# Performance work log

Measured on AMD Instinct MI355X. Metric: run time of the kernel, lower is better.

Reference implementation:

```python
import jax, jax.numpy as jnp
import numpy as np

HID = 101
IN = 3


def lstm_cell(x, h, c, W_ih, W_hh, b_ih, b_hh):
    # PyTorch LSTMCell gate order: i, f, g, o
    gates = x @ W_ih.T + b_ih + h @ W_hh.T + b_hh  # [B, 4H]
    i, f, g, o = jnp.split(gates, 4, axis=-1)
    i = jax.nn.sigmoid(i)
    f = jax.nn.sigmoid(f)
    g = jnp.tanh(g)
    o = jax.nn.sigmoid(o)
    c_new = f * c + i * g
    h_new = o * jnp.tanh(c_new)
    return h_new, c_new


def setup_inputs() -> dict:
    key = jax.random.key(0)
    ks = jax.random.split(key, 12)
    B, T = 1024, 256
    s1 = 1.0 / np.sqrt(HID)
    u = lambda k, shp: jax.random.uniform(k, shp, jnp.float32, -s1, s1)
    return {
        "input": jax.random.normal(ks[0], (B, T, IN), jnp.float32),
        "W_ih1": u(ks[1], (4 * HID, IN)),
        "W_hh1": u(ks[2], (4 * HID, HID)),
        "b_ih1": u(ks[3], (4 * HID,)),
        "b_hh1": u(ks[4], (4 * HID,)),
        "W_ih2": u(ks[5], (4 * HID, HID)),
        "W_hh2": u(ks[6], (4 * HID, HID)),
        "b_ih2": u(ks[7], (4 * HID,)),
        "b_hh2": u(ks[8], (4 * HID,)),
        "Wl": u(ks[9], (IN, HID)),
        "bl": u(ks[10], (IN,)),
        "future": 32,
    }


def reference(input, W_ih1, W_hh1, b_ih1, b_hh1, W_ih2, W_hh2, b_ih2, b_hh2, Wl, bl, future):
    B = input.shape[0]
    h1 = jnp.zeros((B, HID), input.dtype)
    c1 = jnp.zeros((B, HID), input.dtype)
    h2 = jnp.zeros((B, HID), input.dtype)
    c2 = jnp.zeros((B, HID), input.dtype)

    def step(carry, x_t):
        h1, c1, h2, c2 = carry
        h1, c1 = lstm_cell(x_t, h1, c1, W_ih1, W_hh1, b_ih1, b_hh1)
        h2, c2 = lstm_cell(h1, h2, c2, W_ih2, W_hh2, b_ih2, b_hh2)
        out = h2 @ Wl.T + bl  # [B, 3]
        return (h1, c1, h2, c2), out

    xs = jnp.transpose(input, (1, 0, 2))  # [T, B, 3]
    carry, outs = jax.lax.scan(step, (h1, c1, h2, c2), xs)

    if future > 0:
        last_out = outs[-1]

        def fstep(carry, _):
            h1, c1, h2, c2, out = carry
            h1, c1 = lstm_cell(out, h1, c1, W_ih1, W_hh1, b_ih1, b_hh1)
            h2, c2 = lstm_cell(h1, h2, c2, W_ih2, W_hh2, b_ih2, b_hh2)
            out = h2 @ Wl.T + bl
            return (h1, c1, h2, c2, out), out

        _, fouts = jax.lax.scan(fstep, (*carry, last_out), None, length=future)
        outs = jnp.concatenate([outs, fouts], axis=0)

    return jnp.transpose(outs, (1, 0, 2))  # [B, T+future, 3]
```

## Files before the change

kernel.cpp:

```cpp
#include <hip/hip_runtime.h>
#include <hip/hip_bf16.h>

#define HID 101
#define BATCH 1024
#define RPB 4
#define NBLK 256
#define NTHR 512
#define TSEQ 256

#define A1SZ  (7*4*4*512)
#define A2SZ  (7*4*7*512)
#define A2OFF A1SZ
#define AOOFF (A1SZ + A2SZ)
#define AOSZ  (4*512)

typedef _Float16 h8 __attribute__((ext_vector_type(8)));
typedef float f4 __attribute__((ext_vector_type(4)));

__global__ void prep_kernel(const float* __restrict__ W_ih1, const float* __restrict__ W_hh1,
                            const float* __restrict__ b_ih1, const float* __restrict__ b_hh1,
                            const float* __restrict__ W_ih2, const float* __restrict__ W_hh2,
                            const float* __restrict__ b_ih2, const float* __restrict__ b_hh2,
                            const float* __restrict__ Wl, _Float16* __restrict__ wsA) {
    int idx = blockIdx.x * blockDim.x + threadIdx.x;
    int stride = gridDim.x * blockDim.x;
    for (int t = idx; t < A1SZ; t += stride) {
        int i = t & 7, lane = (t >> 3) & 63, kt = (t >> 9) & 3, tau = (t >> 11) & 3, w = t >> 13;
        int k = kt * 32 + ((lane >> 4) & 3) * 8 + i;
        int u = 16 * w + (lane & 15);
        float v = 0.f;
        if (u < HID) {
            int g = tau * HID + u;
            if (k < HID) v = W_hh1[g * HID + k];
            else if (k >= 101 && k <= 103) v = W_ih1[g * 3 + (k - 101)];
            else if (k == 104) v = b_ih1[g] + b_hh1[g];
        }
        wsA[t] = (_Float16)v;
    }
    for (int t = idx; t < A2SZ; t += stride) {
        int i = t & 7, lane = (t >> 3) & 63;
        int rem = t >> 9;
        int kt = rem % 7; rem /= 7;
        int tau = rem & 3, w = rem >> 2;
        int k = kt * 32 + ((lane >> 4) & 3) * 8 + i;
        int u = 16 * w + (lane & 15);
        float v = 0.f;
        if (u < HID) {
            int g = tau * HID + u;
            if (k < HID) v = W_ih2[g * HID + k];
            else if (k == 104) v = b_ih2[g] + b_hh2[g];
            else if (k >= 112 && k < 213) v = W_hh2[g * HID + (k - 112)];
        }
        wsA[A2OFF + t] = (_Float16)v;
    }
    for (int t = idx; t < AOSZ; t += stride) {
        int i = t & 7, lane = (t >> 3) & 63, kk = (t >> 9) & 3;
        int k = (kk + 3) * 32 + ((lane >> 4) & 3) * 8 + i;
        int j = lane & 15;
        float v = (j < 3 && k >= 112 && k < 213) ? Wl[j * HID + (k - 112)] : 0.f;
        wsA[AOOFF + t] = (_Float16)v;
    }
}

__device__ __forceinline__ float sigm(float z) {
    return __builtin_amdgcn_rcpf(1.f + __expf(-z));
}
__device__ __forceinline__ float tanhf_(float z) {
    return 1.f - 2.f * __builtin_amdgcn_rcpf(__expf(2.f * z) + 1.f);
}

#define MFMA(acc, a, b) acc = __builtin_amdgcn_mfma_f32_16x16x32_f16(a, b, acc, 0, 0, 0)

__global__ __launch_bounds__(NTHR, 2) void lstm_kernel(
    const float* __restrict__ input, const _Float16* __restrict__ wsA,
    const float* __restrict__ bl, int steps, float* __restrict__ out)
{
    const int tid = threadIdx.x;
    const int wid = tid >> 6, lane = tid & 63;
    const int q = lane >> 4, col = lane & 15;
    const int r0 = blockIdx.x * RPB;
    const int ostride = steps * 3;

    __shared__ _Float16 Sb[2][3584];
    __shared__ float zwA[7][4][4][16];
    __shared__ float zwB[7][4][4][16];
    __shared__ _Float16 xpre[TSEQ * 12];

    h8 A1[4][4];
    h8 A2[4][7];
    if (wid < 7) {
        #pragma unroll
        for (int tau = 0; tau < 4; tau++) {
            #pragma unroll
            for (int kt = 0; kt < 4; kt++)
                A1[tau][kt] = *(const volatile h8*)(
                    wsA + ((size_t)((wid * 4 + tau) * 4 + kt) * 512 + lane * 8));
            #pragma unroll
            for (int kt = 0; kt < 7; kt++)
                A2[tau][kt] = *(const volatile h8*)(
                    wsA + (size_t)A2OFF + ((size_t)((wid * 4 + tau) * 7 + kt) * 512 + lane * 8));
        }
    } else {
        #pragma unroll
        for (int kt = 0; kt < 4; kt++)
            A2[0][kt] = *(const volatile h8*)(
                wsA + (size_t)AOOFF + ((size_t)(kt) * 512 + lane * 8));
    }
    const float bl0 = bl[0], bl1 = bl[1], bl2 = bl[2];

    const int r_ew = lane & 3, ul = lane >> 2;
    const int u = 16 * wid + ul;
    const bool ewv = (wid < 7) && (u < HID);
    const int slot1 = (u >> 3) * 128 + r_ew * 8 + (u & 7);
    const int slot2 = (14 + (u >> 3)) * 128 + r_ew * 8 + (u & 7);
    const int boff = q * 128 + col * 8;
    const int xr = lane / 3, xj = lane - 3 * xr;
    const int xoff = 12 * 128 + xr * 8 + 5 + xj;

    for (int i2 = tid; i2 < 3584; i2 += NTHR) {
        Sb[0][i2] = (_Float16)0.f; Sb[1][i2] = (_Float16)0.f;
    }
    for (int g = tid; g < RPB * TSEQ * 3; g += NTHR) {
        int r = g / (TSEQ * 3), rem = g - r * (TSEQ * 3);
        int tt = rem / 3, j = rem - 3 * tt;
        xpre[tt * 12 + r * 3 + j] = (_Float16)input[(size_t)(r0 + r) * (TSEQ * 3) + rem];
    }
    __syncthreads();
    if (tid < 16) {
        Sb[0][13 * 128 + tid * 8] = (_Float16)1.0f;
        Sb[1][13 * 128 + tid * 8] = (_Float16)1.0f;
    }
    if (tid < 12) {
        int r = tid / 3, j = tid - 3 * (tid / 3);
        Sb[0][12 * 128 + r * 8 + 5 + j] = xpre[r * 3 + j];
    }
    float c1 = 0.f, c2 = 0.f;
    __syncthreads();

    for (int t = 0; t < TSEQ; ++t) {
        _Float16* Rb = Sb[t & 1];
        _Float16* Wt = Sb[1 - (t & 1)];
        if (wid < 7) {
            h8 bf0 = *(const h8*)(Rb + 0 * 512 + boff);
            h8 bf1 = *(const h8*)(Rb + 1 * 512 + boff);
            h8 bf2 = *(const h8*)(Rb + 2 * 512 + boff);
            h8 bf3 = *(const h8*)(Rb + 3 * 512 + boff);
            h8 bf4 = *(const h8*)(Rb + 4 * 512 + boff);
            h8 bf5 = *(const h8*)(Rb + 5 * 512 + boff);
            h8 bf6 = *(const h8*)(Rb + 6 * 512 + boff);
            f4 a0 = {0.f,0.f,0.f,0.f}, a1 = a0, a2 = a0, a3 = a0;
            MFMA(a0, A1[0][0], bf0); MFMA(a1, A1[1][0], bf0); MFMA(a2, A1[2][0], bf0); MFMA(a3, A1[3][0], bf0);
            MFMA(a0, A1[0][1], bf1); MFMA(a1, A1[1][1], bf1); MFMA(a2, A1[2][1], bf1); MFMA(a3, A1[3][1], bf1);
            MFMA(a0, A1[0][2], bf2); MFMA(a1, A1[1][2], bf2); MFMA(a2, A1[2][2], bf2); MFMA(a3, A1[3][2], bf2);
            MFMA(a0, A1[0][3], bf3); MFMA(a1, A1[1][3], bf3); MFMA(a2, A1[2][3], bf3); MFMA(a3, A1[3][3], bf3);
            if (col < 4) {
                *(f4*)&zwA[wid][0][col][4 * q] = a0;
                *(f4*)&zwA[wid][1][col][4 * q] = a1;
                *(f4*)&zwA[wid][2][col][4 * q] = a2;
                *(f4*)&zwA[wid][3][col][4 * q] = a3;
            }
            if (t >= 1) {
                f4 b0 = {0.f,0.f,0.f,0.f}, b1 = b0, b2 = b0, b3 = b0;
                MFMA(b0, A2[0][0], bf0); MFMA(b1, A2[1][0], bf0); MFMA(b2, A2[2][0], bf0); MFMA(b3, A2[3][0], bf0);
                MFMA(b0, A2[0][1], bf1); MFMA(b1, A2[1][1], bf1); MFMA(b2, A2[2][1], bf1); MFMA(b3, A2[3][1], bf1);
                MFMA(b0, A2[0][2], bf2); MFMA(b1, A2[1][2], bf2); MFMA(b2, A2[2][2], bf2); MFMA(b3, A2[3][2], bf2);
                MFMA(b0, A2[0][3], bf3); MFMA(b1, A2[1][3], bf3); MFMA(b2, A2[2][3], bf3); MFMA(b3, A2[3][3], bf3);
                MFMA(b0, A2[0][4], bf4); MFMA(b1, A2[1][4], bf4); MFMA(b2, A2[2][4], bf4); MFMA(b3, A2[3][4], bf4);
                MFMA(b0, A2[0][5], bf5); MFMA(b1, A2[1][5], bf5); MFMA(b2, A2[2][5], bf5); MFMA(b3, A2[3][5], bf5);
                MFMA(b0, A2[0][6], bf6); MFMA(b1, A2[1][6], bf6); MFMA(b2, A2[2][6], bf6); MFMA(b3, A2[3][6], bf6);
                if (col < 4) {
                    *(f4*)&zwB[wid][0][col][4 * q] = b0;
                    *(f4*)&zwB[wid][1][col][4 * q] = b1;
                    *(f4*)&zwB[wid][2][col][4 * q] = b2;
                    *(f4*)&zwB[wid][3][col][4 * q] = b3;
                }
            }
            {
                float z0 = zwA[wid][0][r_ew][ul], z1 = zwA[wid][1][r_ew][ul];
                float z2 = zwA[wid][2][r_ew][ul], z3 = zwA[wid][3][r_ew][ul];
                float ig = sigm(z0), fg = sigm(z1), gg = tanhf_(z2), og = sigm(z3);
                c1 = fg * c1 + ig * gg;
                float h1v = og * tanhf_(c1);
                if (ewv) Wt[slot1] = (_Float16)h1v;
            }
            if (t >= 1) {
                float z0 = zwB[wid][0][r_ew][ul], z1 = zwB[wid][1][r_ew][ul];
                float z2 = zwB[wid][2][r_ew][ul], z3 = zwB[wid][3][r_ew][ul];
                float ig = sigm(z0), fg = sigm(z1), gg = tanhf_(z2), og = sigm(z3);
                c2 = fg * c2 + ig * gg;
                float h2v = og * tanhf_(c2);
                if (ewv) Wt[slot2] = (_Float16)h2v;
            }
        } else {
            if (t >= 2) {
                f4 ao = {0.f, 0.f, 0.f, 0.f};
                #pragma unroll
                for (int kk = 0; kk < 4; kk++) {
                    h8 b = (_Float16)0.f;
                    if (col < 4) b = *(const h8*)(Rb + (kk + 3) * 512 + boff);
                    MFMA(ao, A2[0][kk], b);
                }
                if (lane < 4) {
                    float* op = out + (size_t)(r0 + lane) * ostride + (size_t)(t - 2) * 3;
                    op[0] = ao[0] + bl0; op[1] = ao[1] + bl1; op[2] = ao[2] + bl2;
                }
            }
            if (t + 1 < TSEQ && lane < 12)
                Wt[xoff] = xpre[(t + 1) * 12 + xr * 3 + xj];
        }
        __syncthreads();
    }

    {
        _Float16* Rb = Sb[0];
        _Float16* Wt = Sb[1];
        if (wid < 7) {
            h8 bf0 = *(const h8*)(Rb + 0 * 512 + boff);
            h8 bf1 = *(const h8*)(Rb + 1 * 512 + boff);
            h8 bf2 = *(const h8*)(Rb + 2 * 512 + boff);
            h8 bf3 = *(const h8*)(Rb + 3 * 512 + boff);
            h8 bf4 = *(const h8*)(Rb + 4 * 512 + boff);
            h8 bf5 = *(const h8*)(Rb + 5 * 512 + boff);
            h8 bf6 = *(const h8*)(Rb + 6 * 512 + boff);
            f4 b0 = {0.f,0.f,0.f,0.f}, b1 = b0, b2 = b0, b3 = b0;
            MFMA(b0, A2[0][0], bf0); MFMA(b1, A2[1][0], bf0); MFMA(b2, A2[2][0], bf0); MFMA(b3, A2[3][0], bf0);
            MFMA(b0, A2[0][1], bf1); MFMA(b1, A2[1][1], bf1); MFMA(b2, A2[2][1], bf1); MFMA(b3, A2[3][1], bf1);
            MFMA(b0, A2[0][2], bf2); MFMA(b1, A2[1][2], bf2); MFMA(b2, A2[2][2], bf2); MFMA(b3, A2[3][2], bf2);
            MFMA(b0, A2[0][3], bf3); MFMA(b1, A2[1][3], bf3); MFMA(b2, A2[2][3], bf3); MFMA(b3, A2[3][3], bf3);
            MFMA(b0, A2[0][4], bf4); MFMA(b1, A2[1][4], bf4); MFMA(b2, A2[2][4], bf4); MFMA(b3, A2[3][4], bf4);
            MFMA(b0, A2[0][5], bf5); MFMA(b1, A2[1][5], bf5); MFMA(b2, A2[2][5], bf5); MFMA(b3, A2[3][5], bf5);
            MFMA(b0, A2[0][6], bf6); MFMA(b1, A2[1][6], bf6); MFMA(b2, A2[2][6], bf6); MFMA(b3, A2[3][6], bf6);
            if (col < 4) {
                *(f4*)&zwB[wid][0][col][4 * q] = b0;
                *(f4*)&zwB[wid][1][col][4 * q] = b1;
                *(f4*)&zwB[wid][2][col][4 * q] = b2;
                *(f4*)&zwB[wid][3][col][4 * q] = b3;
            }
            float z0 = zwB[wid][0][r_ew][ul], z1 = zwB[wid][1][r_ew][ul];
            float z2 = zwB[wid][2][r_ew][ul], z3 = zwB[wid][3][r_ew][ul];
            float ig = sigm(z0), fg = sigm(z1), gg = tanhf_(z2), og = sigm(z3);
            c2 = fg * c2 + ig * gg;
            float h2v = og * tanhf_(c2);
            if (ewv) Wt[slot2] = (_Float16)h2v;
        } else {
            f4 ao = {0.f, 0.f, 0.f, 0.f};
            #pragma unroll
            for (int kk = 0; kk < 4; kk++) {
                h8 b = (_Float16)0.f;
                if (col < 4) b = *(const h8*)(Rb + (kk + 3) * 512 + boff);
                MFMA(ao, A2[0][kk], b);
            }
            if (lane < 4) {
                float* op = out + (size_t)(r0 + lane) * ostride + (size_t)(TSEQ - 2) * 3;
                op[0] = ao[0] + bl0; op[1] = ao[1] + bl1; op[2] = ao[2] + bl2;
            }
        }
        __syncthreads();
    }

    for (int t = TSEQ; t < steps; ++t) {
        _Float16* R = Sb[t & 1];
        _Float16* W = Sb[1 - (t & 1)];
        if (wid == 7) {
            f4 ao = {0.f, 0.f, 0.f, 0.f};
            #pragma unroll
            for (int kk = 0; kk < 4; kk++) {
                h8 b = (_Float16)0.f;
                if (col < 4) b = *(const h8*)(W + (kk + 3) * 512 + boff);
                MFMA(ao, A2[0][kk], b);
            }
            if (lane < 4) {
                float o0 = ao[0] + bl0, o1 = ao[1] + bl1, o2 = ao[2] + bl2;
                float* op = out + (size_t)(r0 + lane) * ostride + (size_t)(t - 1) * 3;
                op[0] = o0; op[1] = o1; op[2] = o2;
                R[12 * 128 + lane * 8 + 5] = (_Float16)o0;
                R[12 * 128 + lane * 8 + 6] = (_Float16)o1;
                R[12 * 128 + lane * 8 + 7] = (_Float16)o2;
            }
        }
        __syncthreads();
        if (wid < 7) {
            f4 a0 = {0.f,0.f,0.f,0.f}, a1 = a0, a2 = a0, a3 = a0;
            #pragma unroll
            for (int kt = 0; kt < 4; kt++) {
                h8 b = (_Float16)0.f;
                if (col < 4) b = *(const h8*)(R + kt * 512 + boff);
                MFMA(a0, A1[0][kt], b); MFMA(a1, A1[1][kt], b);
                MFMA(a2, A1[2][kt], b); MFMA(a3, A1[3][kt], b);
            }
            if (col < 4) {
                *(f4*)&zwA[wid][0][col][4 * q] = a0;
                *(f4*)&zwA[wid][1][col][4 * q] = a1;
                *(f4*)&zwA[wid][2][col][4 * q] = a2;
                *(f4*)&zwA[wid][3][col][4 * q] = a3;
            }
            float z0 = zwA[wid][0][r_ew][ul], z1 = zwA[wid][1][r_ew][ul];
            float z2 = zwA[wid][2][r_ew][ul], z3 = zwA[wid][3][r_ew][ul];
            float ig = sigm(z0), fg = sigm(z1), gg = tanhf_(z2), og = sigm(z3);
            c1 = fg * c1 + ig * gg;
            float h1v = og * tanhf_(c1);
            if (ewv) W[slot1] = (_Float16)h1v;
        }
        __syncthreads();
        if (wid < 7) {
            f4 b0 = {0.f,0.f,0.f,0.f}, b1 = b0, b2 = b0, b3 = b0;
            #pragma unroll
            for (int kt = 0; kt < 7; kt++) {
                h8 b = (_Float16)0.f;
                if (col < 4) b = *(const h8*)(W + kt * 512 + boff);
                MFMA(b0, A2[0][kt], b); MFMA(b1, A2[1][kt], b);
                MFMA(b2, A2[2][kt], b); MFMA(b3, A2[3][kt], b);
            }
            if (col < 4) {
                *(f4*)&zwB[wid][0][col][4 * q] = b0;
                *(f4*)&zwB[wid][1][col][4 * q] = b1;
                *(f4*)&zwB[wid][2][col][4 * q] = b2;
                *(f4*)&zwB[wid][3][col][4 * q] = b3;
            }
            float z0 = zwB[wid][0][r_ew][ul], z1 = zwB[wid][1][r_ew][ul];
            float z2 = zwB[wid][2][r_ew][ul], z3 = zwB[wid][3][r_ew][ul];
            float ig = sigm(z0), fg = sigm(z1), gg = tanhf_(z2), og = sigm(z3);
            c2 = fg * c2 + ig * gg;
            float h2v = og * tanhf_(c2);
            if (ewv) R[slot2] = (_Float16)h2v;
        }
        __syncthreads();
    }

    if (wid == 7) {
        f4 ao = {0.f, 0.f, 0.f, 0.f};
        #pragma unroll
        for (int kk = 0; kk < 4; kk++) {
            h8 b = (_Float16)0.f;
            if (col < 4) b = *(const h8*)(&Sb[1][0] + (kk + 3) * 512 + boff);
            MFMA(ao, A2[0][kk], b);
        }
        if (lane < 4) {
            float* op = out + (size_t)(r0 + lane) * ostride + (size_t)(steps - 1) * 3;
            op[0] = ao[0] + bl0; op[1] = ao[1] + bl1; op[2] = ao[2] + bl2;
        }
    }
}

extern "C" void kernel_launch(void* const* d_in, const int* in_sizes, int n_in,
                              void* d_out, int out_size, void* d_ws, size_t ws_size,
                              hipStream_t stream) {
    const float* input = (const float*)d_in[0];
    const float* W_ih1 = (const float*)d_in[1];
    const float* W_hh1 = (const float*)d_in[2];
    const float* b_ih1 = (const float*)d_in[3];
    const float* b_hh1 = (const float*)d_in[4];
    const float* W_ih2 = (const float*)d_in[5];
    const float* W_hh2 = (const float*)d_in[6];
    const float* b_ih2 = (const float*)d_in[7];
    const float* b_hh2 = (const float*)d_in[8];
    const float* Wl    = (const float*)d_in[9];
    const float* bl    = (const float*)d_in[10];
    int steps = out_size / (BATCH * 3);
    _Float16* wsA = (_Float16*)d_ws;

    hipLaunchKernelGGL(prep_kernel, dim3(512), dim3(256), 0, stream,
                       W_ih1, W_hh1, b_ih1, b_hh1, W_ih2, W_hh2, b_ih2, b_hh2, Wl, wsA);
    hipLaunchKernelGGL(lstm_kernel, dim3(NBLK), dim3(NTHR), 0, stream,
                       input, wsA, bl, steps, (float*)d_out);
}
```

Before: 425.4 us.

## Split gate MFMA work across 16 waves and separate layer elementwise waves

Doubles the block to 1024 threads, so each of 14 MFMA waves computes two of the four gate tiles per layer instead of all four. Layer-1 and layer-2 elementwise updates are now done by separate wave groups, with an added barrier between the MFMA phase and the elementwise phase. The aim is to shorten the serial per-step critical path by halving each wave's MFMA chain and halving the per-wave weight registers. In exchange it drops the two-blocks-per-CU launch bound and adds a block-wide barrier each timestep.

After: 524.5 us. 1.23x slower.

```diff
diff --git a/kernel.cpp b/kernel.cpp
--- a/kernel.cpp
+++ b/kernel.cpp
@@ -5,7 +5,7 @@
 #define BATCH 1024
 #define RPB 4
 #define NBLK 256
-#define NTHR 512
+#define NTHR 1024
 #define TSEQ 256
 
 #define A1SZ  (7*4*4*512)
@@ -71,7 +71,7 @@
 
 #define MFMA(acc, a, b) acc = __builtin_amdgcn_mfma_f32_16x16x32_f16(a, b, acc, 0, 0, 0)
 
-__global__ __launch_bounds__(NTHR, 2) void lstm_kernel(
+__global__ __launch_bounds__(NTHR) void lstm_kernel(
     const float* __restrict__ input, const _Float16* __restrict__ wsA,
     const float* __restrict__ bl, int steps, float* __restrict__ out)
 {
@@ -81,36 +81,42 @@
     const int r0 = blockIdx.x * RPB;
     const int ostride = steps * 3;
 
+    const int w = wid & 7;
+    const bool mfmaw = (w < 7) && (wid != 7);
+    const int tb = (wid < 8) ? 0 : 2;
+
     __shared__ _Float16 Sb[2][3584];
     __shared__ float zwA[7][4][4][16];
     __shared__ float zwB[7][4][4][16];
     __shared__ _Float16 xpre[TSEQ * 12];
 
-    h8 A1[4][4];
-    h8 A2[4][7];
-    if (wid < 7) {
+    h8 A1[2][4];
+    h8 A2[2][7];
+    h8 AO[4];
+    if (mfmaw) {
         #pragma unroll
-        for (int tau = 0; tau < 4; tau++) {
+        for (int tt = 0; tt < 2; tt++) {
             #pragma unroll
             for (int kt = 0; kt < 4; kt++)
-                A1[tau][kt] = *(const volatile h8*)(
-                    wsA + ((size_t)((wid * 4 + tau) * 4 + kt) * 512 + lane * 8));
+                A1[tt][kt] = *(const volatile h8*)(
+                    wsA + ((size_t)((w * 4 + tb + tt) * 4 + kt) * 512 + lane * 8));
             #pragma unroll
             for (int kt = 0; kt < 7; kt++)
-                A2[tau][kt] = *(const volatile h8*)(
-                    wsA + (size_t)A2OFF + ((size_t)((wid * 4 + tau) * 7 + kt) * 512 + lane * 8));
-        }
-    } else {
+                A2[tt][kt] = *(const volatile h8*)(
+                    wsA + (size_t)A2OFF + ((size_t)((w * 4 + tb + tt) * 7 + kt) * 512 + lane * 8));
+        }
+    } else if (wid == 7) {
         #pragma unroll
         for (int kt = 0; kt < 4; kt++)
-            A2[0][kt] = *(const volatile h8*)(
+            AO[kt] = *(const volatile h8*)(
                 wsA + (size_t)AOOFF + ((size_t)(kt) * 512 + lane * 8));
     }
     const float bl0 = bl[0], bl1 = bl[1], bl2 = bl[2];
 
     const int r_ew = lane & 3, ul = lane >> 2;
-    const int u = 16 * wid + ul;
-    const bool ewv = (wid < 7) && (u < HID);
+    const int uw = (wid < 8) ? wid : (wid - 8);
+    const int u = 16 * uw + ul;
+    const bool ewv = (uw < 7) && (u < HID);
     const int slot1 = (u >> 3) * 128 + r_ew * 8 + (u & 7);
     const int slot2 = (14 + (u >> 3)) * 128 + r_ew * 8 + (u & 7);
     const int boff = q * 128 + col * 8;
@@ -140,70 +146,54 @@
     for (int t = 0; t < TSEQ; ++t) {
         _Float16* Rb = Sb[t & 1];
         _Float16* Wt = Sb[1 - (t & 1)];
+        f4 ao = {0.f, 0.f, 0.f, 0.f};
+        if (mfmaw) {
+            f4 a0 = {0.f,0.f,0.f,0.f}, a1 = a0, b0 = a0, b1 = a0;
+            #pragma unroll
+            for (int kt = 0; kt < 7; kt++) {
+                h8 bf = (_Float16)0.f;
+                if (col < 4) bf = *(const h8*)(Rb + kt * 512 + boff);
+                if (kt < 4) { MFMA(a0, A1[0][kt], bf); MFMA(a1, A1[1][kt], bf); }
+                if (t >= 1) { MFMA(b0, A2[0][kt], bf); MFMA(b1, A2[1][kt], bf); }
+            }
+            if (col < 4) {
+                *(f4*)&zwA[w][tb + 0][col][4 * q] = a0;
+                *(f4*)&zwA[w][tb + 1][col][4 * q] = a1;
+                if (t >= 1) {
+                    *(f4*)&zwB[w][tb + 0][col][4 * q] = b0;
+                    *(f4*)&zwB[w][tb + 1][col][4 * q] = b1;
+                }
+            }
+        } else if (wid == 7 && t >= 2) {
+            #pragma unroll
+            for (int kk = 0; kk < 4; kk++) {
+                h8 bf = (_Float16)0.f;
+                if (col < 4) bf = *(const h8*)(Rb + (kk + 3) * 512 + boff);
+                MFMA(ao, AO[kk], bf);
+            }
+        }
+        __syncthreads();
         if (wid < 7) {
-            h8 bf0 = *(const h8*)(Rb + 0 * 512 + boff);
-            h8 bf1 = *(const h8*)(Rb + 1 * 512 + boff);
-            h8 bf2 = *(const h8*)(Rb + 2 * 512 + boff);
-            h8 bf3 = *(const h8*)(Rb + 3 * 512 + boff);
-            h8 bf4 = *(const h8*)(Rb + 4 * 512 + boff);
-            h8 bf5 = *(const h8*)(Rb + 5 * 512 + boff);
-            h8 bf6 = *(const h8*)(Rb + 6 * 512 + boff);
-            f4 a0 = {0.f,0.f,0.f,0.f}, a1 = a0, a2 = a0, a3 = a0;
-            MFMA(a0, A1[0][0], bf0); MFMA(a1, A1[1][0], bf0); MFMA(a2, A1[2][0], bf0); MFMA(a3, A1[3][0], bf0);
-            MFMA(a0, A1[0][1], bf1); MFMA(a1, A1[1][1], bf1); MFMA(a2, A1[2][1], bf1); MFMA(a3, A1[3][1], bf1);
-            MFMA(a0, A1[0][2], bf2); MFMA(a1, A1[1][2], bf2); MFMA(a2, A1[2][2], bf2); MFMA(a3, A1[3][2], bf2);
-            MFMA(a0, A1[0][3], bf3); MFMA(a1, A1[1][3], bf3); MFMA(a2, A1[2][3], bf3); MFMA(a3, A1[3][3], bf3);
-            if (col < 4) {
-                *(f4*)&zwA[wid][0][col][4 * q] = a0;
-                *(f4*)&zwA[wid][1][col][4 * q] = a1;
-                *(f4*)&zwA[wid][2][col][4 * q] = a2;
-                *(f4*)&zwA[wid][3][col][4 * q] = a3;
-            }
+            float z0 = zwA[wid][0][r_ew][ul], z1 = zwA[wid][1][r_ew][ul];
+            float z2 = zwA[wid][2][r_ew][ul], z3 = zwA[wid][3][r_ew][ul];
+            float ig = sigm(z0), fg = sigm(z1), gg = tanhf_(z2), og = sigm(z3);
+            c1 = fg * c1 + ig * gg;
+            float h1v = og * tanhf_(c1);
+            if (ewv) Wt[slot1] = (_Float16)h1v;
+        } else if (wid >= 8 && wid < 15) {
             if (t >= 1) {
-                f4 b0 = {0.f,0.f,0.f,0.f}, b1 = b0, b2 = b0, b3 = b0;
-                MFMA(b0, A2[0][0], bf0); MFMA(b1, A2[1][0], bf0); MFMA(b2, A2[2][0], bf0); MFMA(b3, A2[3][0], bf0);
-                MFMA(b0, A2[0][1], bf1); MFMA(b1, A2[1][1], bf1); MFMA(b2, A2[2][1], bf1); MFMA(b3, A2[3][1], bf1);
-                MFMA(b0, A2[0][2], bf2); MFMA(b1, A2[1][2], bf2); MFMA(b2, A2[2][2], bf2); MFMA(b3, A2[3][2], bf2);
-                MFMA(b0, A2[0][3], bf3); MFMA(b1, A2[1][3], bf3); MFMA(b2, A2[2][3], bf3); MFMA(b3, A2[3][3], bf3);
-                MFMA(b0, A2[0][4], bf4); MFMA(b1, A2[1][4], bf4); MFMA(b2, A2[2][4], bf4); MFMA(b3, A2[3][4], bf4);
-                MFMA(b0, A2[0][5], bf5); MFMA(b1, A2[1][5], bf5); MFMA(b2, A2[2][5], bf5); MFMA(b3, A2[3][5], bf5);
-                MFMA(b0, A2[0][6], bf6); MFMA(b1, A2[1][6], bf6); MFMA(b2, A2[2][6], bf6); MFMA(b3, A2[3][6], bf6);
-                if (col < 4) {
-                    *(f4*)&zwB[wid][0][col][4 * q] = b0;
-                    *(f4*)&zwB[wid][1][col][4 * q] = b1;
-                    *(f4*)&zwB[wid][2][col][4 * q] = b2;
-                    *(f4*)&zwB[wid][3][col][4 * q] = b3;
-                }
-            }
-            {
-                float z0 = zwA[wid][0][r_ew][ul], z1 = zwA[wid][1][r_ew][ul];
-                float z2 = zwA[wid][2][r_ew][ul], z3 = zwA[wid][3][r_ew][ul];
-                float ig = sigm(z0), fg = sigm(z1), gg = tanhf_(z2), og = sigm(z3);
-                c1 = fg * c1 + ig * gg;
-                float h1v = og * tanhf_(c1);
-                if (ewv) Wt[slot1] = (_Float16)h1v;
-            }
-            if (t >= 1) {
-                float z0 = zwB[wid][0][r_ew][ul], z1 = zwB[wid][1][r_ew][ul];
-                float z2 = zwB[wid][2][r_ew][ul], z3 = zwB[wid][3][r_ew][ul];
+                int w2 = wid - 8;
+                float z0 = zwB[w2][0][r_ew][ul], z1 = zwB[w2][1][r_ew][ul];
+                float z2 = zwB[w2][2][r_ew][ul], z3 = zwB[w2][3][r_ew][ul];
                 float ig = sigm(z0), fg = sigm(z1), gg = tanhf_(z2), og = sigm(z3);
                 c2 = fg * c2 + ig * gg;
                 float h2v = og * tanhf_(c2);
                 if (ewv) Wt[slot2] = (_Float16)h2v;
             }
-        } else {
-            if (t >= 2) {
-                f4 ao = {0.f, 0.f, 0.f, 0.f};
-                #pragma unroll
-                for (int kk = 0; kk < 4; kk++) {
-                    h8 b = (_Float16)0.f;
-                    if (col < 4) b = *(const h8*)(Rb + (kk + 3) * 512 + boff);
-                    MFMA(ao, A2[0][kk], b);
-                }
-                if (lane < 4) {
-                    float* op = out + (size_t)(r0 + lane) * ostride + (size_t)(t - 2) * 3;
-                    op[0] = ao[0] + bl0; op[1] = ao[1] + bl1; op[2] = ao[2] + bl2;
-                }
+        } else if (wid == 7) {
+            if (t >= 2 && lane < 4) {
+                float* op = out + (size_t)(r0 + lane) * ostride + (size_t)(t - 2) * 3;
+                op[0] = ao[0] + bl0; op[1] = ao[1] + bl1; op[2] = ao[2] + bl2;
             }
             if (t + 1 < TSEQ && lane < 12)
                 Wt[xoff] = xpre[(t + 1) * 12 + xr * 3 + xj];
@@ -214,46 +204,39 @@
     {
         _Float16* Rb = Sb[0];
         _Float16* Wt = Sb[1];
-        if (wid < 7) {
-            h8 bf0 = *(const h8*)(Rb + 0 * 512 + boff);
-            h8 bf1 = *(const h8*)(Rb + 1 * 512 + boff);
-            h8 bf2 = *(const h8*)(Rb + 2 * 512 + boff);
-            h8 bf3 = *(const h8*)(Rb + 3 * 512 + boff);
-            h8 bf4 = *(const h8*)(Rb + 4 * 512 + boff);
-            h8 bf5 = *(const h8*)(Rb + 5 * 512 + boff);
-            h8 bf6 = *(const h8*)(Rb + 6 * 512 + boff);
-            f4 b0 = {0.f,0.f,0.f,0.f}, b1 = b0, b2 = b0, b3 = b0;
-            MFMA(b0, A2[0][0], bf0); MFMA(b1, A2[1][0], bf0); MFMA(b2, A2[2][0], bf0); MFMA(b3, A2[3][0], bf0);
-            MFMA(b0, A2[0][1], bf1); MFMA(b1, A2[1][1], bf1); MFMA(b2, A2[2][1], bf1); MFMA(b3, A2[3][1], bf1);
-            MFMA(b0, A2[0][2], bf2); MFMA(b1, A2[1][2], bf2); MFMA(b2, A2[2][2], bf2); MFMA(b3, A2[3][2], bf2);
-            MFMA(b0, A2[0][3], bf3); MFMA(b1, A2[1][3], bf3); MFMA(b2, A2[2][3], bf3); MFMA(b3, A2[3][3], bf3);
-            MFMA(b0, A2[0][4], bf4); MFMA(b1, A2[1][4], bf4); MFMA(b2, A2[2][4], bf4); MFMA(b3, A2[3][4], bf4);
-            MFMA(b0, A2[0][5], bf5); MFMA(b1, A2[1][5], bf5); MFMA(b2, A2[2][5], bf5); MFMA(b3, A2[3][5], bf5);
-            MFMA(b0, A2[0][6], bf6); MFMA(b1, A2[1][6], bf6); MFMA(b2, A2[2][6], bf6); MFMA(b3, A2[3][6], bf6);
+        f4 ao = {0.f, 0.f, 0.f, 0.f};
+        if (mfmaw) {
+            f4 b0 = {0.f,0.f,0.f,0.f}, b1 = b0;
+            #pragma unroll
+            for (int kt = 0; kt < 7; kt++) {
+                h8 bf = (_Float16)0.f;
+                if (col < 4) bf = *(const h8*)(Rb + kt * 512 + boff);
+                MFMA(b0, A2[0][kt], bf); MFMA(b1, A2[1][kt], bf);
+            }
             if (col < 4) {
-                *(f4*)&zwB[wid][0][col][4 * q] = b0;
-                *(f4*)&zwB[wid][1][col][4 * q] = b1;
-                *(f4*)&zwB[wid][2][col][4 * q] = b2;
-                *(f4*)&zwB[wid][3][col][4 * q] = b3;
-            }
-            float z0 = zwB[wid][0][r_ew][ul], z1 = zwB[wid][1][r_ew][ul];
-            float z2 = zwB[wid][2][r_ew][ul], z3 = zwB[wid][3][r_ew][ul];
+                *(f4*)&zwB[w][tb + 0][col][4 * q] = b0;
+                *(f4*)&zwB[w][tb + 1][col][4 * q] = b1;
+            }
+        } else if (wid == 7) {
+            #pragma unroll
+            for (int kk = 0; kk < 4; kk++) {
+                h8 bf = (_Float16)0.f;
+                if (col < 4) bf = *(const h8*)(Rb + (kk + 3) * 512 + boff);
+                MFMA(ao, AO[kk], bf);
+            }
+        }
+        __syncthreads();
+        if (wid >= 8 && wid < 15) {
+            int w2 = wid - 8;
+            float z0 = zwB[w2][0][r_ew][ul], z1 = zwB[w2][1][r_ew][ul];
+            float z2 = zwB[w2][2][r_ew][ul], z3 = zwB[w2][3][r_ew][ul];
             float ig = sigm(z0), fg = sigm(z1), gg = tanhf_(z2), og = sigm(z3);
             c2 = fg * c2 + ig * gg;
             float h2v = og * tanhf_(c2);
             if (ewv) Wt[slot2] = (_Float16)h2v;
-        } else {
-            f4 ao = {0.f, 0.f, 0.f, 0.f};
-            #pragma unroll
-            for (int kk = 0; kk < 4; kk++) {
-                h8 b = (_Float16)0.f;
-                if (col < 4) b = *(const h8*)(Rb + (kk + 3) * 512 + boff);
-                MFMA(ao, A2[0][kk], b);
-            }
-            if (lane < 4) {
-                float* op = out + (size_t)(r0 + lane) * ostride + (size_t)(TSEQ - 2) * 3;
-                op[0] = ao[0] + bl0; op[1] = ao[1] + bl1; op[2] = ao[2] + bl2;
-            }
+        } else if (wid == 7 && lane < 4) {
+            float* op = out + (size_t)(r0 + lane) * ostride + (size_t)(TSEQ - 2) * 3;
+            op[0] = ao[0] + bl0; op[1] = ao[1] + bl1; op[2] = ao[2] + bl2;
         }
         __syncthreads();
     }
@@ -265,9 +248,9 @@
             f4 ao = {0.f, 0.f, 0.f, 0.f};
             #pragma unroll
             for (int kk = 0; kk < 4; kk++) {
-                h8 b = (_Float16)0.f;
-                if (col < 4) b = *(const h8*)(W + (kk + 3) * 512 + boff);
-                MFMA(ao, A2[0][kk], b);
+                h8 bf = (_Float16)0.f;
+                if (col < 4) bf = *(const h8*)(W + (kk + 3) * 512 + boff);
+                MFMA(ao, AO[kk], bf);
             }
             if (lane < 4) {
                 float o0 = ao[0] + bl0, o1 = ao[1] + bl1, o2 = ao[2] + bl2;
@@ -279,21 +262,21 @@
             }
         }
         __syncthreads();
+        if (mfmaw) {
+            f4 a0 = {0.f,0.f,0.f,0.f}, a1 = a0;
+            #pragma unroll
+            for (int kt = 0; kt < 4; kt++) {
+                h8 bf = (_Float16)0.f;
+                if (col < 4) bf = *(const h8*)(R + kt * 512 + boff);
+                MFMA(a0, A1[0][kt], bf); MFMA(a1, A1[1][kt], bf);
+            }
+            if (col < 4) {
+                *(f4*)&zwA[w][tb + 0][col][4 * q] = a0;
+                *(f4*)&zwA[w][tb + 1][col][4 * q] = a1;
+            }
+        }
+        __syncthreads();
         if (wid < 7) {
-            f4 a0 = {0.f,0.f,0.f,0.f}, a1 = a0, a2 = a0, a3 = a0;
-            #pragma unroll
-            for (int kt = 0; kt < 4; kt++) {
-                h8 b = (_Float16)0.f;
-                if (col < 4) b = *(const h8*)(R + kt * 512 + boff);
-                MFMA(a0, A1[0][kt], b); MFMA(a1, A1[1][kt], b);
-                MFMA(a2, A1[2][kt], b); MFMA(a3, A1[3][kt], b);
-            }
-            if (col < 4) {
-                *(f4*)&zwA[wid][0][col][4 * q] = a0;
-                *(f4*)&zwA[wid][1][col][4 * q] = a1;
-                *(f4*)&zwA[wid][2][col][4 * q] = a2;
-                *(f4*)&zwA[wid][3][col][4 * q] = a3;
-            }
             float z0 = zwA[wid][0][r_ew][ul], z1 = zwA[wid][1][r_ew][ul];
             float z2 = zwA[wid][2][r_ew][ul], z3 = zwA[wid][3][r_ew][ul];
             float ig = sigm(z0), fg = sigm(z1), gg = tanhf_(z2), og = sigm(z3);
@@ -302,23 +285,24 @@
             if (ewv) W[slot1] = (_Float16)h1v;
         }
         __syncthreads();
-        if (wid < 7) {
-            f4 b0 = {0.f,0.f,0.f,0.f}, b1 = b0, b2 = b0, b3 = b0;
+        if (mfmaw) {
+            f4 b0 = {0.f,0.f,0.f,0.f}, b1 = b0;
             #pragma unroll
             for (int kt = 0; kt < 7; kt++) {
-                h8 b = (_Float16)0.f;
-                if (col < 4) b = *(const h8*)(W + kt * 512 + boff);
-                MFMA(b0, A2[0][kt], b); MFMA(b1, A2[1][kt], b);
-                MFMA(b2, A2[2][kt], b); MFMA(b3, A2[3][kt], b);
+                h8 bf = (_Float16)0.f;
+                if (col < 4) bf = *(const h8*)(W + kt * 512 + boff);
+                MFMA(b0, A2[0][kt], bf); MFMA(b1, A2[1][kt], bf);
             }
             if (col < 4) {
-                *(f4*)&zwB[wid][0][col][4 * q] = b0;
-                *(f4*)&zwB[wid][1][col][4 * q] = b1;
-                *(f4*)&zwB[wid][2][col][4 * q] = b2;
-                *(f4*)&zwB[wid][3][col][4 * q] = b3;
-            }
-            float z0 = zwB[wid][0][r_ew][ul], z1 = zwB[wid][1][r_ew][ul];
-            float z2 = zwB[wid][2][r_ew][ul], z3 = zwB[wid][3][r_ew][ul];
+                *(f4*)&zwB[w][tb + 0][col][4 * q] = b0;
+                *(f4*)&zwB[w][tb + 1][col][4 * q] = b1;
+            }
+        }
+        __syncthreads();
+        if (wid >= 8 && wid < 15) {
+            int w2 = wid - 8;
+            float z0 = zwB[w2][0][r_ew][ul], z1 = zwB[w2][1][r_ew][ul];
+            float z2 = zwB[w2][2][r_ew][ul], z3 = zwB[w2][3][r_ew][ul];
             float ig = sigm(z0), fg = sigm(z1), gg = tanhf_(z2), og = sigm(z3);
             c2 = fg * c2 + ig * gg;
             float h2v = og * tanhf_(c2);
@@ -331,9 +315,9 @@
         f4 ao = {0.f, 0.f, 0.f, 0.f};
         #pragma unroll
         for (int kk = 0; kk < 4; kk++) {
-            h8 b = (_Float16)0.f;
-            if (col < 4) b = *(const h8*)(&Sb[1][0] + (kk + 3) * 512 + boff);
-            MFMA(ao, A2[0][kk], b);
+            h8 bf = (_Float16)0.f;
+            if (col < 4) bf = *(const h8*)(&Sb[1][0] + (kk + 3) * 512 + boff);
+            MFMA(ao, AO[kk], bf);
         }
         if (lane < 4) {
             float* op = out + (size_t)(r0 + lane) * ostride + (size_t)(steps - 1) * 3;
```
